# Performance work log

Measured on AMD Instinct MI355X. Metric: run time of the kernel, lower is better.

Reference implementation:

```python
import jax, jax.numpy as jnp
import numpy as np

EPS = 1e-6


def setup_inputs() -> dict:
    key = jax.random.key(0)
    k1, k2, k3, k4 = jax.random.split(key, 4)
    B, H, J, K = 32, 8, 8192, 128
    memory = jax.random.normal(k1, (B, J, K), dtype=jnp.float32)
    keys = jax.random.normal(k2, (B, H, K), dtype=jnp.float32)
    strengths = jax.random.normal(k3, (B, H, 1), dtype=jnp.float32)
    mask = jax.random.uniform(k4, (B, H, K), dtype=jnp.float32)
    return {"memory": memory, "keys": keys, "strengths": strengths, "mask": mask}


def reference(memory, keys, strengths, mask):
    # Faithful math: masked_keys = mask*keys; masked_memory[i,h,j,k] = mask[i,h,k]*memory[i,j,k]
    # projections[i,h,j] = sum_k mask^2 * keys * memory  (mask appears in both operands)
    # We fold mask^2 into the contractions to avoid materializing [i,h,j,k].
    mask2 = mask * mask                                   # [B,H,K]
    projections = jnp.einsum('ihk,ijk->ihj', mask2 * keys, memory)
    keys_norm = jnp.linalg.norm(mask * keys, axis=-1)     # [B,H]
    # ||masked_memory||[i,h,j] = sqrt(sum_k mask^2 * memory^2)
    memory_norm = jnp.sqrt(jnp.einsum('ihk,ijk->ihj', mask2, memory * memory))
    norm = keys_norm[..., None] * memory_norm             # [B,H,J]
    similarity = projections / (norm + EPS)
    sharp = similarity * jax.nn.softplus(strengths)       # strengths [B,H,1] broadcasts
    return jax.nn.softmax(sharp, axis=-1)
```

## Files before the change

### kernel.cpp

```cpp
#include <hip/hip_runtime.h>
#include <math.h>

constexpr int B_ = 32;
constexpr int H_ = 8;
constexpr int J_ = 8192;
constexpr int K_ = 128;
constexpr float EPS_ = 1e-6f;

constexpr int SBLK = 64;
constexpr int JPB  = J_ / SBLK;
constexpr int ITERS = JPB / 16;

template <int CTRL>
__device__ __forceinline__ float dpp_add(float x) {
  int v = __builtin_amdgcn_update_dpp(0, __float_as_int(x), CTRL, 0xF, 0xF, true);
  return x + __int_as_float(v);
}

__device__ __forceinline__ float red16(float x) {
  x = dpp_add<0xB1>(x);
  x = dpp_add<0x4E>(x);
  x = dpp_add<0x141>(x);
  x = dpp_add<0x140>(x);
  return x;
}

__device__ __forceinline__ float dot4f(const float4 a, const float4 b, float acc) {
  acc = fmaf(a.x, b.x, acc);
  acc = fmaf(a.y, b.y, acc);
  acc = fmaf(a.z, b.z, acc);
  acc = fmaf(a.w, b.w, acc);
  return acc;
}

__global__ __launch_bounds__(256, 2) void cw_main(
    const float* __restrict__ memory, const float* __restrict__ keys,
    const float* __restrict__ strengths, const float* __restrict__ mask,
    float* __restrict__ out)
{
  const int bid  = blockIdx.x;
  const int i    = bid / SBLK;
  const int jb   = bid % SBLK;
  const int t    = threadIdx.x;
  const int wave = t >> 6;
  const int lane = t & 63;
  const int grp  = lane >> 4;
  const int sub  = lane & 15;
  const int myh  = sub & 7;

  const float4* keyv = (const float4*)(keys + (size_t)i * H_ * K_);
  const float4* mskv = (const float4*)(mask + (size_t)i * H_ * K_);
  float4 cA[H_][2];
  float4 cB[H_][2];
  float kn[H_];
  #pragma unroll
  for (int h = 0; h < H_; ++h) {
    float knp = 0.0f;
    #pragma unroll
    for (int c = 0; c < 2; ++c) {
      const float4 kv = keyv[h * 32 + c * 16 + sub];
      const float4 mv = mskv[h * 32 + c * 16 + sub];
      float4 b, a;
      b.x = mv.x * mv.x; b.y = mv.y * mv.y; b.z = mv.z * mv.z; b.w = mv.w * mv.w;
      a.x = b.x * kv.x;  a.y = b.y * kv.y;  a.z = b.z * kv.z;  a.w = b.w * kv.w;
      cB[h][c] = b;
      cA[h][c] = a;
      knp = dot4f(a, kv, knp);
    }
    kn[h] = red16(knp);
  }
  float kn2 = kn[0];
  #pragma unroll
  for (int h = 1; h < H_; ++h) if (myh == h) kn2 = kn[h];
  const float knorm = sqrtf(kn2);
  const float st = strengths[i * H_ + myh];
  const float sp = fmaxf(st, 0.0f) + log1pf(expf(-fabsf(st)));

  const int j0 = jb * JPB + wave * 4 + grp;
  const float4* rowv = (const float4*)(memory + ((size_t)i * J_ + j0) * K_);

  float4 m0 = rowv[sub];
  float4 m1 = rowv[sub + 16];

  #pragma unroll 1
  for (int it = 0; it < ITERS; ++it) {
    const int nx = (it + 1 < ITERS) ? (it + 1) : 0;
    const float4* nr = rowv + (size_t)nx * 512;
    const float4 n0v = nr[sub];
    const float4 n1v = nr[sub + 16];

    float4 sq0, sq1;
    sq0.x = m0.x * m0.x; sq0.y = m0.y * m0.y; sq0.z = m0.z * m0.z; sq0.w = m0.w * m0.w;
    sq1.x = m1.x * m1.x; sq1.y = m1.y * m1.y; sq1.z = m1.z * m1.z; sq1.w = m1.w * m1.w;

    float p[H_], nn[H_];
    #pragma unroll
    for (int h = 0; h < H_; ++h) {
      float a = m0.x * cA[h][0].x;
      a = fmaf(m0.y, cA[h][0].y, a);
      a = fmaf(m0.z, cA[h][0].z, a);
      a = fmaf(m0.w, cA[h][0].w, a);
      a = dot4f(m1, cA[h][1], a);
      p[h] = a;
      float b = sq0.x * cB[h][0].x;
      b = fmaf(sq0.y, cB[h][0].y, b);
      b = fmaf(sq0.z, cB[h][0].z, b);
      b = fmaf(sq0.w, cB[h][0].w, b);
      b = dot4f(sq1, cB[h][1], b);
      nn[h] = b;
    }

    #pragma unroll
    for (int h = 0; h < H_; ++h) {
      p[h]  = red16(p[h]);
      nn[h] = red16(nn[h]);
    }

    if (sub < 8) {
      float pp = p[0], qq = nn[0];
      #pragma unroll
      for (int h = 1; h < H_; ++h) {
        if (myh == h) { pp = p[h]; qq = nn[h]; }
      }
      const float mnorm = sqrtf(qq);
      const float sharp = pp / (knorm * mnorm + EPS_) * sp;
      const int j = jb * JPB + it * 16 + wave * 4 + grp;
      out[((size_t)(i * H_ + myh)) * J_ + j] = sharp;
    }

    m0 = n0v;
    m1 = n1v;
  }
}

__global__ __launch_bounds__(256) void cw_softmax(float* __restrict__ out)
{
  const int row = blockIdx.x;
  float4* pv = (float4*)(out + (size_t)row * J_);
  const int t = threadIdx.x;
  const int wave = t >> 6, lane = t & 63;

  float4 v[8];
  float mx = -3.4e38f;
  #pragma unroll
  for (int c = 0; c < 8; ++c) {
    v[c] = pv[t + c * 256];
    mx = fmaxf(mx, fmaxf(fmaxf(v[c].x, v[c].y), fmaxf(v[c].z, v[c].w)));
  }
  #pragma unroll
  for (int o = 32; o > 0; o >>= 1) mx = fmaxf(mx, __shfl_xor(mx, o, 64));
  __shared__ float sm[4];
  __shared__ float ss[4];
  if (lane == 0) sm[wave] = mx;
  __syncthreads();
  mx = fmaxf(fmaxf(sm[0], sm[1]), fmaxf(sm[2], sm[3]));

  float sum = 0.0f;
  #pragma unroll
  for (int c = 0; c < 8; ++c) {
    v[c].x = expf(v[c].x - mx);
    v[c].y = expf(v[c].y - mx);
    v[c].z = expf(v[c].z - mx);
    v[c].w = expf(v[c].w - mx);
    sum += (v[c].x + v[c].y) + (v[c].z + v[c].w);
  }
  #pragma unroll
  for (int o = 32; o > 0; o >>= 1) sum += __shfl_xor(sum, o, 64);
  if (lane == 0) ss[wave] = sum;
  __syncthreads();
  sum = (ss[0] + ss[1]) + (ss[2] + ss[3]);
  const float inv = 1.0f / sum;

  #pragma unroll
  for (int c = 0; c < 8; ++c) {
    v[c].x *= inv; v[c].y *= inv; v[c].z *= inv; v[c].w *= inv;
    pv[t + c * 256] = v[c];
  }
}

extern "C" void kernel_launch(void* const* d_in, const int* in_sizes, int n_in,
                              void* d_out, int out_size, void* d_ws, size_t ws_size,
                              hipStream_t stream) {
  const float* memory    = (const float*)d_in[0];
  const float* keys      = (const float*)d_in[1];
  const float* strengths = (const float*)d_in[2];
  const float* mask      = (const float*)d_in[3];
  float* out = (float*)d_out;

  (void)d_ws; (void)ws_size;

  cw_main<<<B_ * SBLK, 256, 0, stream>>>(memory, keys, strengths, mask, out);
  cw_softmax<<<B_ * H_, 256, 0, stream>>>(out);
}
```

Baseline: 209.0 us.

## Split heads across wave pairs to cut registers and raise occupancy

Each wave now handles 4 of the 8 heads for 8 rows per iteration, instead of all 8 heads for 16 rows. This halves the per-thread key/mask constant registers and allows launch bounds of 4 blocks per CU for better latency hiding. The cost is that each memory row is loaded by two waves, doubling global/cache traffic. The softmax kernel is also reshaped to 1024 threads per row with two float4s per thread and a shuffle-based cross-wave reduction.

After: 206.5 us, median of 2. About the same (-1.2%).

```diff
diff --git a/kernel.cpp b/kernel.cpp
--- a/kernel.cpp
+++ b/kernel.cpp
@@ -9,7 +9,8 @@
 
 constexpr int SBLK = 64;
 constexpr int JPB  = J_ / SBLK;
-constexpr int ITERS = JPB / 16;
+constexpr int RPI  = 8;
+constexpr int ITERS = JPB / RPI;
 
 template <int CTRL>
 __device__ __forceinline__ float dpp_add(float x) {
@@ -33,28 +34,31 @@
   return acc;
 }
 
-__global__ __launch_bounds__(256, 2) void cw_main(
+__global__ __launch_bounds__(256, 4) void cw_main(
     const float* __restrict__ memory, const float* __restrict__ keys,
     const float* __restrict__ strengths, const float* __restrict__ mask,
     float* __restrict__ out)
 {
   const int bid  = blockIdx.x;
-  const int i    = bid / SBLK;
-  const int jb   = bid % SBLK;
+  const int i    = bid >> 6;
+  const int jb   = bid & 63;
   const int t    = threadIdx.x;
   const int wave = t >> 6;
   const int lane = t & 63;
   const int grp  = lane >> 4;
   const int sub  = lane & 15;
-  const int myh  = sub & 7;
+  const int hs   = (wave >> 1) << 2;
+  const int hl   = sub & 3;
+  const int myh  = hs + hl;
 
   const float4* keyv = (const float4*)(keys + (size_t)i * H_ * K_);
   const float4* mskv = (const float4*)(mask + (size_t)i * H_ * K_);
-  float4 cA[H_][2];
-  float4 cB[H_][2];
-  float kn[H_];
+  float4 cA[4][2];
+  float4 cB[4][2];
+  float kn[4];
   #pragma unroll
-  for (int h = 0; h < H_; ++h) {
+  for (int hh = 0; hh < 4; ++hh) {
+    const int h = hs + hh;
     float knp = 0.0f;
     #pragma unroll
     for (int c = 0; c < 2; ++c) {
@@ -63,20 +67,21 @@
       float4 b, a;
       b.x = mv.x * mv.x; b.y = mv.y * mv.y; b.z = mv.z * mv.z; b.w = mv.w * mv.w;
       a.x = b.x * kv.x;  a.y = b.y * kv.y;  a.z = b.z * kv.z;  a.w = b.w * kv.w;
-      cB[h][c] = b;
-      cA[h][c] = a;
+      cB[hh][c] = b;
+      cA[hh][c] = a;
       knp = dot4f(a, kv, knp);
     }
-    kn[h] = red16(knp);
+    kn[hh] = red16(knp);
   }
   float kn2 = kn[0];
   #pragma unroll
-  for (int h = 1; h < H_; ++h) if (myh == h) kn2 = kn[h];
+  for (int hh = 1; hh < 4; ++hh) if (hl == hh) kn2 = kn[hh];
   const float knorm = sqrtf(kn2);
   const float st = strengths[i * H_ + myh];
   const float sp = fmaxf(st, 0.0f) + log1pf(expf(-fabsf(st)));
 
-  const int j0 = jb * JPB + wave * 4 + grp;
+  const int jrow0 = (wave & 1) * 4 + grp;
+  const int j0    = jb * JPB + jrow0;
   const float4* rowv = (const float4*)(memory + ((size_t)i * J_ + j0) * K_);
 
   float4 m0 = rowv[sub];
@@ -85,7 +90,7 @@
   #pragma unroll 1
   for (int it = 0; it < ITERS; ++it) {
     const int nx = (it + 1 < ITERS) ? (it + 1) : 0;
-    const float4* nr = rowv + (size_t)nx * 512;
+    const float4* nr = rowv + (size_t)nx * 256;
     const float4 n0v = nr[sub];
     const float4 n1v = nr[sub + 16];
 
@@ -93,38 +98,38 @@
     sq0.x = m0.x * m0.x; sq0.y = m0.y * m0.y; sq0.z = m0.z * m0.z; sq0.w = m0.w * m0.w;
     sq1.x = m1.x * m1.x; sq1.y = m1.y * m1.y; sq1.z = m1.z * m1.z; sq1.w = m1.w * m1.w;
 
-    float p[H_], nn[H_];
+    float p[4], nn[4];
     #pragma unroll
-    for (int h = 0; h < H_; ++h) {
-      float a = m0.x * cA[h][0].x;
-      a = fmaf(m0.y, cA[h][0].y, a);
-      a = fmaf(m0.z, cA[h][0].z, a);
-      a = fmaf(m0.w, cA[h][0].w, a);
-      a = dot4f(m1, cA[h][1], a);
-      p[h] = a;
-      float b = sq0.x * cB[h][0].x;
-      b = fmaf(sq0.y, cB[h][0].y, b);
-      b = fmaf(sq0.z, cB[h][0].z, b);
-      b = fmaf(sq0.w, cB[h][0].w, b);
-      b = dot4f(sq1, cB[h][1], b);
-      nn[h] = b;
+    for (int hh = 0; hh < 4; ++hh) {
+      float a = m0.x * cA[hh][0].x;
+      a = fmaf(m0.y, cA[hh][0].y, a);
+      a = fmaf(m0.z, cA[hh][0].z, a);
+      a = fmaf(m0.w, cA[hh][0].w, a);
+      a = dot4f(m1, cA[hh][1], a);
+      p[hh] = a;
+      float b = sq0.x * cB[hh][0].x;
+      b = fmaf(sq0.y, cB[hh][0].y, b);
+      b = fmaf(sq0.z, cB[hh][0].z, b);
+      b = fmaf(sq0.w, cB[hh][0].w, b);
+      b = dot4f(sq1, cB[hh][1], b);
+      nn[hh] = b;
     }
 
     #pragma unroll
-    for (int h = 0; h < H_; ++h) {
-      p[h]  = red16(p[h]);
-      nn[h] = red16(nn[h]);
+    for (int hh = 0; hh < 4; ++hh) {
+      p[hh]  = red16(p[hh]);
+      nn[hh] = red16(nn[hh]);
     }
 
-    if (sub < 8) {
+    if (sub < 4) {
       float pp = p[0], qq = nn[0];
       #pragma unroll
-      for (int h = 1; h < H_; ++h) {
-        if (myh == h) { pp = p[h]; qq = nn[h]; }
+      for (int hh = 1; hh < 4; ++hh) {
+        if (hl == hh) { pp = p[hh]; qq = nn[hh]; }
       }
       const float mnorm = sqrtf(qq);
       const float sharp = pp / (knorm * mnorm + EPS_) * sp;
-      const int j = jb * JPB + it * 16 + wave * 4 + grp;
+      const int j = jb * JPB + it * RPI + jrow0;
       out[((size_t)(i * H_ + myh)) * J_ + j] = sharp;
     }
 
@@ -133,49 +138,45 @@
   }
 }
 
-__global__ __launch_bounds__(256) void cw_softmax(float* __restrict__ out)
+__global__ __launch_bounds__(1024) void cw_softmax(float* __restrict__ out)
 {
   const int row = blockIdx.x;
   float4* pv = (float4*)(out + (size_t)row * J_);
   const int t = threadIdx.x;
   const int wave = t >> 6, lane = t & 63;
 
-  float4 v[8];
-  float mx = -3.4e38f;
-  #pragma unroll
-  for (int c = 0; c < 8; ++c) {
-    v[c] = pv[t + c * 256];
-    mx = fmaxf(mx, fmaxf(fmaxf(v[c].x, v[c].y), fmaxf(v[c].z, v[c].w)));
-  }
+  float4 v0 = pv[t];
+  float4 v1 = pv[t + 1024];
+  float mx = fmaxf(fmaxf(fmaxf(v0.x, v0.y), fmaxf(v0.z, v0.w)),
+                   fmaxf(fmaxf(v1.x, v1.y), fmaxf(v1.z, v1.w)));
   #pragma unroll
   for (int o = 32; o > 0; o >>= 1) mx = fmaxf(mx, __shfl_xor(mx, o, 64));
-  __shared__ float sm[4];
-  __shared__ float ss[4];
+  __shared__ float sm[16];
+  __shared__ float ss[16];
   if (lane == 0) sm[wave] = mx;
   __syncthreads();
-  mx = fmaxf(fmaxf(sm[0], sm[1]), fmaxf(sm[2], sm[3]));
+  mx = sm[lane & 15];
+  #pragma unroll
+  for (int o = 8; o > 0; o >>= 1) mx = fmaxf(mx, __shfl_xor(mx, o, 64));
 
-  float sum = 0.0f;
-  #pragma unroll
-  for (int c = 0; c < 8; ++c) {
-    v[c].x = expf(v[c].x - mx);
-    v[c].y = expf(v[c].y - mx);
-    v[c].z = expf(v[c].z - mx);
-    v[c].w = expf(v[c].w - mx);
-    sum += (v[c].x + v[c].y) + (v[c].z + v[c].w);
-  }
+  v0.x = expf(v0.x - mx); v0.y = expf(v0.y - mx);
+  v0.z = expf(v0.z - mx); v0.w = expf(v0.w - mx);
+  v1.x = expf(v1.x - mx); v1.y = expf(v1.y - mx);
+  v1.z = expf(v1.z - mx); v1.w = expf(v1.w - mx);
+  float sum = ((v0.x + v0.y) + (v0.z + v0.w)) + ((v1.x + v1.y) + (v1.z + v1.w));
   #pragma unroll
   for (int o = 32; o > 0; o >>= 1) sum += __shfl_xor(sum, o, 64);
   if (lane == 0) ss[wave] = sum;
   __syncthreads();
-  sum = (ss[0] + ss[1]) + (ss[2] + ss[3]);
+  sum = ss[lane & 15];
+  #pragma unroll
+  for (int o = 8; o > 0; o >>= 1) sum += __shfl_xor(sum, o, 64);
   const float inv = 1.0f / sum;
 
-  #pragma unroll
-  for (int c = 0; c < 8; ++c) {
-    v[c].x *= inv; v[c].y *= inv; v[c].z *= inv; v[c].w *= inv;
-    pv[t + c * 256] = v[c];
-  }
+  v0.x *= inv; v0.y *= inv; v0.z *= inv; v0.w *= inv;
+  v1.x *= inv; v1.y *= inv; v1.z *= inv; v1.w *= inv;
+  pv[t] = v0;
+  pv[t + 1024] = v1;
 }
 
 extern "C" void kernel_launch(void* const* d_in, const int* in_sizes, int n_in,
@@ -190,5 +191,5 @@
   (void)d_ws; (void)ws_size;
 
   cw_main<<<B_ * SBLK, 256, 0, stream>>>(memory, keys, strengths, mask, out);
-  cw_softmax<<<B_ * H_, 256, 0, stream>>>(out);
+  cw_softmax<<<B_ * H_, 1024, 0, stream>>>(out);
 }
```
